# Kernel optimization log

Hardware: AMD Instinct MI355X
Metric: run time of the kernel (lower is better)

## Reference

```python
import jax, jax.numpy as jnp
import numpy as np

B, S, D, H, HD, L, V = 32, 512, 512, 8, 64, 6, 64000
EPS = 1e-5

def _layer_norm(x, g, b):
    mu = jnp.mean(x, axis=-1, keepdims=True)
    var = jnp.mean(jnp.square(x - mu), axis=-1, keepdims=True)
    return (x - mu) * jax.lax.rsqrt(var + EPS) * g + b

def _sinusoidal_pe():
    pos = np.arange(S)[:, None].astype(np.float32)
    div = np.exp(np.arange(0, D, 2).astype(np.float32) * -(np.log(10000.0) / D))
    pe = np.zeros((S, D), dtype=np.float32)
    pe[:, 0::2] = np.sin(pos * div)
    pe[:, 1::2] = np.cos(pos * div)
    return jnp.asarray(pe)

def setup_inputs() -> dict:
    key = jax.random.key(0)
    ks = jax.random.split(key, 8)
    std = 0.02
    return {
        'tokens': jax.random.randint(ks[0], (B, S), 0, V),
        'mask': jnp.ones((B, S), dtype=jnp.int32),
        'emb': jax.random.normal(ks[1], (V, D), jnp.float32) * std,
        'pe': _sinusoidal_pe(),
        'Wq': jax.random.normal(ks[2], (L, H, D, HD), jnp.float32) * std,
        'Wk': jax.random.normal(ks[3], (L, H, D, HD), jnp.float32) * std,
        'Wv': jax.random.normal(ks[4], (L, H, D, HD), jnp.float32) * std,
        'Wo': jax.random.normal(ks[5], (L, D, D), jnp.float32) * std,
        'ln1_g': jnp.ones((L, D), jnp.float32),
        'ln1_b': jnp.zeros((L, D), jnp.float32),
        'W1': jax.random.normal(ks[6], (L, D, 4 * D), jnp.float32) * std,
        'b1': jnp.zeros((L, 4 * D), jnp.float32),
        'W2': jax.random.normal(ks[7], (L, 4 * D, D), jnp.float32) * std,
        'b2': jnp.zeros((L, D), jnp.float32),
        'ln2_g': jnp.ones((L, D), jnp.float32),
        'ln2_b': jnp.zeros((L, D), jnp.float32),
    }

def reference(tokens, mask, emb, pe, Wq, Wk, Wv, Wo, ln1_g, ln1_b, W1, b1, W2, b2, ln2_g, ln2_b):
    # Eval mode: all dropouts are identity.
    x = emb[tokens] + pe[None, :S, :]               # [B,S,D]
    neg_inf = jnp.finfo(x.dtype).min
    mask_b = (mask == 0)[:, None, None, :]          # [B,1,1,S] broadcast over heads & queries
    scale = HD ** -0.5
    for l in range(L):
        q = jnp.einsum('bsd,hde->bhse', x, Wq[l])
        k = jnp.einsum('bsd,hde->bhse', x, Wk[l])
        v = jnp.einsum('bsd,hde->bhse', x, Wv[l])
        w = jnp.einsum('bhse,bhte->bhst', q, k) * scale
        w = jnp.where(mask_b, neg_inf, w)
        a = jax.nn.softmax(w, axis=-1)
        o = jnp.einsum('bhst,bhte->bhse', a, v)     # [B,H,S,HD]
        o = o.transpose(0, 2, 1, 3).reshape(x.shape[0], S, D)  # concat heads
        x = _layer_norm(x + o @ Wo[l], ln1_g[l], ln1_b[l])
        h = jax.nn.gelu(x @ W1[l] + b1[l], approximate=False) @ W2[l] + b2[l]
        x = _layer_norm(x + h, ln2_g[l], ln2_b[l])
    return x
```

## Files before the change

### kernel.cpp

```cpp
#include <hip/hip_runtime.h>

#define BB 32
#define SS 512
#define DD 512
#define HH 8
#define HDH 64
#define LL 6
#define DFF 2048
#define MM (BB*SS)

typedef __attribute__((ext_vector_type(4))) float f32x4;
typedef __attribute__((ext_vector_type(8))) short s16x8;
typedef __attribute__((ext_vector_type(4))) short s16x4;

__device__ __forceinline__ unsigned short f2bf(float f) {
    union { float f; unsigned u; } v; v.f = f;
    unsigned r = v.u + 0x7fffu + ((v.u >> 16) & 1u);
    return (unsigned short)(r >> 16);
}
__device__ __forceinline__ float bf2f(unsigned short b) {
    union { unsigned u; float f; } v; v.u = ((unsigned)b) << 16;
    return v.f;
}

__device__ __forceinline__ f32x4 mfma_bf16(s16x8 a, s16x8 b, f32x4 c) {
    asm("v_mfma_f32_16x16x32_bf16 %0, %1, %2, %0" : "+v"(c) : "v"(a), "v"(b));
    return c;
}

__device__ __forceinline__ void gload_lds16(const void* g, void* l) {
    __builtin_amdgcn_global_load_lds(
        (__attribute__((address_space(1))) void*)g,
        (__attribute__((address_space(3))) void*)l, 16, 0, 0);
}

__global__ __launch_bounds__(256) void k_conv_qkv3(const float* __restrict__ Wq,
                                                   const float* __restrict__ Wk,
                                                   const float* __restrict__ Wv,
                                                   unsigned short* __restrict__ dst) {
    int i = blockIdx.x * 256 + threadIdx.x;
    if (i >= LL*3*DD*DD) return;
    int l = i / (3*DD*DD);
    int rem = i - l*(3*DD*DD);
    int n = rem >> 9;
    int kk = rem & 511;
    int which = n >> 9;
    int h = (n >> 6) & 7, e = n & 63;
    const float* W = which == 0 ? Wq : (which == 1 ? Wk : Wv);
    dst[i] = f2bf(W[(((size_t)l*HH + h)*DD + kk)*HDH + e]);
}

__global__ __launch_bounds__(256) void k_conv_t(const float* __restrict__ src,
                                                unsigned short* __restrict__ dst,
                                                int logK, int logN) {
    int i = blockIdx.x * 256 + threadIdx.x;
    if (i >= (LL << (logK + logN))) return;
    int l = i >> (logK + logN);
    int n = (i >> logK) & ((1 << logN) - 1);
    int kk = i & ((1 << logK) - 1);
    dst[i] = f2bf(src[((size_t)l << (logK + logN)) + ((size_t)kk << logN) + n]);
}

__global__ __launch_bounds__(256) void k_embed(const int* __restrict__ tokens,
                                               const float* __restrict__ emb,
                                               const float* __restrict__ pe,
                                               float* __restrict__ x,
                                               unsigned short* __restrict__ xh) {
    int i = blockIdx.x * 256 + threadIdx.x;
    int row = i >> 7;
    int d4 = (i & 127) * 4;
    int srow = row & (SS - 1);
    int tok = tokens[row];
    f32x4 ev = *(const f32x4*)(emb + (size_t)tok*DD + d4);
    f32x4 pv = *(const f32x4*)(pe + (size_t)srow*DD + d4);
    f32x4 vv; s16x4 hv;
    #pragma unroll
    for (int j = 0; j < 4; ++j) {
        vv[j] = ev[j] + pv[j];
        hv[j] = (short)f2bf(vv[j]);
    }
    *(f32x4*)(x + (size_t)row*DD + d4) = vv;
    *(s16x4*)(xh + (size_t)row*DD + d4) = hv;
}

__global__ __launch_bounds__(128) void k_ln(const float* __restrict__ x,
                                            const float* __restrict__ y,
                                            const float* __restrict__ gg,
                                            const float* __restrict__ bb,
                                            float* __restrict__ xo,
                                            unsigned short* __restrict__ xh) {
    const int row = blockIdx.x;
    const int tid = threadIdx.x;
    __shared__ float red[4];
    f32x4 xv = *(const f32x4*)(x + (size_t)row*DD + tid*4);
    f32x4 yv = *(const f32x4*)(y + (size_t)row*DD + tid*4);
    f32x4 vv;
    #pragma unroll
    for (int j = 0; j < 4; ++j) vv[j] = xv[j] + yv[j];
    float sum = vv[0] + vv[1] + vv[2] + vv[3];
    #pragma unroll
    for (int off = 1; off < 64; off <<= 1) sum += __shfl_xor(sum, off);
    if ((tid & 63) == 0) red[tid >> 6] = sum;
    __syncthreads();
    float mu = (red[0] + red[1]) * (1.0f / 512.0f);
    float s2 = 0.0f;
    #pragma unroll
    for (int j = 0; j < 4; ++j) { float d = vv[j] - mu; s2 += d * d; }
    #pragma unroll
    for (int off = 1; off < 64; off <<= 1) s2 += __shfl_xor(s2, off);
    if ((tid & 63) == 0) red[2 + (tid >> 6)] = s2;
    __syncthreads();
    float var = (red[2] + red[3]) * (1.0f / 512.0f);
    float rs = rsqrtf(var + 1e-5f);
    f32x4 gv = *(const f32x4*)(gg + tid*4);
    f32x4 bv = *(const f32x4*)(bb + tid*4);
    f32x4 ov; s16x4 hv;
    #pragma unroll
    for (int j = 0; j < 4; ++j) {
        float o = (vv[j] - mu) * rs * gv[j] + bv[j];
        ov[j] = o;
        hv[j] = (short)f2bf(o);
    }
    *(f32x4*)(xo + (size_t)row*DD + tid*4) = ov;
    *(s16x4*)(xh + (size_t)row*DD + tid*4) = hv;
}

template<int EPI>
__global__ __launch_bounds__(256, 2) void k_gemm(
    const unsigned short* __restrict__ A, const unsigned short* __restrict__ Bt,
    unsigned short* __restrict__ ob, float* __restrict__ of,
    const float* __restrict__ bias, int N, int K, int nt)
{
    __shared__ short lds[2][2][4096];
    const int tid = threadIdx.x;
    const int lane = tid & 63;
    const int wid = tid >> 6;
    const int g = lane >> 4;
    const int t16 = lane & 15;

    int nwg = gridDim.x;
    int bid = blockIdx.x;
    int cpx = nwg >> 3;
    int swz = (bid & 7) * cpx + (bid >> 3);
    int bm = swz / nt;
    int bn = swz - bm * nt;

    const unsigned short* Ag = A  + (size_t)bm * 128 * K;
    const unsigned short* Bg = Bt + (size_t)bn * 128 * K;

    auto stage = [&](int buf, int k0) {
        #pragma unroll
        for (int i = 0; i < 2; ++i) {
            int slot = i * 256 + tid;
            int r = slot >> 2;
            int j = slot & 3;
            int js = j ^ ((r >> 1) & 3);
            size_t go = (size_t)r * K + k0 + js * 8;
            int lo = i * 2048 + wid * 512;
            gload_lds16(Ag + go, &lds[buf][0][lo]);
            gload_lds16(Bg + go, &lds[buf][1][lo]);
        }
    };

    f32x4 acc[4][4];
    #pragma unroll
    for (int a_ = 0; a_ < 4; ++a_)
        #pragma unroll
        for (int b_ = 0; b_ < 4; ++b_) acc[a_][b_] = (f32x4){0.f, 0.f, 0.f, 0.f};

    const int wm = wid >> 1, wn = wid & 1;
    stage(0, 0);
    __syncthreads();
    int nk = K >> 5;
    int buf = 0;
    for (int kt = 0; kt < nk; ++kt) {
        if (kt + 1 < nk) stage(buf ^ 1, (kt + 1) << 5);
        s16x8 af[4], bf_[4];
        #pragma unroll
        for (int mt = 0; mt < 4; ++mt) {
            int r = wm * 64 + mt * 16 + t16;
            af[mt] = *(const s16x8*)&lds[buf][0][r * 32 + ((g ^ ((r >> 1) & 3)) << 3)];
        }
        #pragma unroll
        for (int nt_ = 0; nt_ < 4; ++nt_) {
            int r = wn * 64 + nt_ * 16 + t16;
            bf_[nt_] = *(const s16x8*)&lds[buf][1][r * 32 + ((g ^ ((r >> 1) & 3)) << 3)];
        }
        #pragma unroll
        for (int mt = 0; mt < 4; ++mt)
            #pragma unroll
            for (int nt_ = 0; nt_ < 4; ++nt_)
                acc[mt][nt_] = mfma_bf16(af[mt], bf_[nt_], acc[mt][nt_]);
        __syncthreads();
        buf ^= 1;
    }

    #pragma unroll
    for (int mt = 0; mt < 4; ++mt)
        #pragma unroll
        for (int nt_ = 0; nt_ < 4; ++nt_) {
            int row0 = bm * 128 + wm * 64 + mt * 16 + g * 4;
            int col  = bn * 128 + wn * 64 + nt_ * 16 + t16;
            f32x4 v = acc[mt][nt_];
            float bv = (EPI == 2 || EPI == 3) ? bias[col] : 0.0f;
            #pragma unroll
            for (int r_ = 0; r_ < 4; ++r_) {
                size_t idx = (size_t)(row0 + r_) * N + col;
                if (EPI == 0) {
                    ob[idx] = f2bf(v[r_]);
                } else if (EPI == 1) {
                    of[idx] = v[r_];
                } else if (EPI == 2) {
                    float tv = v[r_] + bv;
                    float ge = 0.5f * tv * (1.0f + erff(tv * 0.70710678118f));
                    ob[idx] = f2bf(ge);
                } else {
                    of[idx] = v[r_] + bv;
                }
            }
        }
}

__global__ __launch_bounds__(1024, 4) void k_attn(
    const unsigned short* __restrict__ qkv, const int* __restrict__ mask,
    unsigned short* __restrict__ o)
{
    extern __shared__ short smem[];
    short* Kl = smem;
    short* Vl = smem + 32768;
    const int tid = threadIdx.x;
    const int lane = tid & 63, wid = tid >> 6;
    short* Pl = smem + 65536 + wid * 1024;
    const int b = blockIdx.x >> 3, h = blockIdx.x & 7;
    const unsigned short* base = qkv + (size_t)b * SS * 1536;
    const int qc = h * 64, kc = 512 + h * 64, vc = 1024 + h * 64;

    for (int c = tid; c < 4096; c += 1024) {
        int t = c >> 3, j = c & 7;
        s16x8 kv = *(const s16x8*)(base + (size_t)t * 1536 + kc + j * 8);
        *(s16x8*)(Kl + t * 64 + ((j ^ (t & 7)) << 3)) = kv;
    }
    {
        int unit = tid >> 1, half = tid & 1;
        int t0 = (unit >> 3) << 3, e0 = (unit & 7) << 3;
        s16x8 r0 = *(const s16x8*)(base + (size_t)(t0 + half*4 + 0) * 1536 + vc + e0);
        s16x8 r1 = *(const s16x8*)(base + (size_t)(t0 + half*4 + 1) * 1536 + vc + e0);
        s16x8 r2 = *(const s16x8*)(base + (size_t)(t0 + half*4 + 2) * 1536 + vc + e0);
        s16x8 r3 = *(const s16x8*)(base + (size_t)(t0 + half*4 + 3) * 1536 + vc + e0);
        #pragma unroll
        for (int j = 0; j < 8; ++j) {
            int e = e0 + j;
            int slot = (t0 >> 3) ^ (e & 7) ^ ((e >> 3) & 7);
            s16x4 w = (s16x4){r0[j], r1[j], r2[j], r3[j]};
            *(s16x4*)(Vl + e * 512 + (slot << 3) + (half << 2)) = w;
        }
    }
    const int g = lane >> 4, t16 = lane & 15;
    unsigned mbits = 0;
    for (int n2 = 0; n2 < 32; ++n2)
        if (mask[b * SS + n2 * 16 + t16] != 0) mbits |= (1u << n2);
    __syncthreads();

    for (int qi = 0; qi < 2; ++qi) {
        const int q0 = (wid * 2 + qi) * 16;
        s16x8 aq[2];
        #pragma unroll
        for (int ks = 0; ks < 2; ++ks)
            aq[ks] = *(const s16x8*)(base + (size_t)(q0 + t16) * 1536 + qc + ks * 32 + g * 8);

        f32x4 oacc[4];
        #pragma unroll
        for (int eo = 0; eo < 4; ++eo) oacc[eo] = (f32x4){0.f, 0.f, 0.f, 0.f};
        float mx[4] = {-3.0e38f, -3.0e38f, -3.0e38f, -3.0e38f};
        float ls[4] = {0.f, 0.f, 0.f, 0.f};

        for (int tc = 0; tc < 4; ++tc) {
            f32x4 s[8];
            #pragma unroll
            for (int n2 = 0; n2 < 8; ++n2) s[n2] = (f32x4){0.f, 0.f, 0.f, 0.f};
            #pragma unroll
            for (int n2 = 0; n2 < 8; ++n2) {
                int t = tc * 128 + n2 * 16 + t16;
                #pragma unroll
                for (int ks = 0; ks < 2; ++ks) {
                    int blk = ks * 4 + g;
                    s16x8 bk = *(const s16x8*)(Kl + t * 64 + ((blk ^ (t & 7)) << 3));
                    s[n2] = mfma_bf16(aq[ks], bk, s[n2]);
                }
            }
            #pragma unroll
            for (int n2 = 0; n2 < 8; ++n2) {
                bool val = (mbits >> (tc * 8 + n2)) & 1u;
                #pragma unroll
                for (int r_ = 0; r_ < 4; ++r_)
                    s[n2][r_] = val ? s[n2][r_] * 0.125f : -3.0e38f;
            }
            float sc[4];
            #pragma unroll
            for (int r_ = 0; r_ < 4; ++r_) {
                float m = s[0][r_];
                #pragma unroll
                for (int n2 = 1; n2 < 8; ++n2) m = fmaxf(m, s[n2][r_]);
                #pragma unroll
                for (int off = 1; off < 16; off <<= 1) m = fmaxf(m, __shfl_xor(m, off));
                float mn = fmaxf(mx[r_], m);
                sc[r_] = __expf(mx[r_] - mn);
                mx[r_] = mn;
                ls[r_] *= sc[r_];
            }
            #pragma unroll
            for (int eo = 0; eo < 4; ++eo)
                #pragma unroll
                for (int r_ = 0; r_ < 4; ++r_) oacc[eo][r_] *= sc[r_];
            #pragma unroll
            for (int n2 = 0; n2 < 8; ++n2)
                #pragma unroll
                for (int r_ = 0; r_ < 4; ++r_)
                    s[n2][r_] = __expf(s[n2][r_] - mx[r_]);
            #pragma unroll
            for (int r_ = 0; r_ < 4; ++r_) {
                float t = 0.f;
                #pragma unroll
                for (int n2 = 0; n2 < 8; ++n2) t += s[n2][r_];
                #pragma unroll
                for (int off = 1; off < 16; off <<= 1) t += __shfl_xor(t, off);
                ls[r_] += t;
            }
            #pragma unroll
            for (int c4 = 0; c4 < 2; ++c4) {
                #pragma unroll
                for (int k4 = 0; k4 < 4; ++k4) {
                    int n2 = c4 * 4 + k4;
                    #pragma unroll
                    for (int r_ = 0; r_ < 4; ++r_) {
                        int qq = g * 4 + r_;
                        int kk = k4 * 16 + t16;
                        Pl[qq * 64 + (((kk >> 3) ^ (qq & 7)) << 3) + (kk & 7)] =
                            (short)f2bf(s[n2][r_]);
                    }
                }
                #pragma unroll
                for (int ks2 = 0; ks2 < 2; ++ks2) {
                    int kk = ks2 * 32 + g * 8;
                    s16x8 pa = *(const s16x8*)(Pl + t16 * 64 + (((kk >> 3) ^ (t16 & 7)) << 3));
                    int tg = tc * 128 + c4 * 64 + kk;
                    #pragma unroll
                    for (int eo = 0; eo < 4; ++eo) {
                        int e = eo * 16 + t16;
                        int slot = (tg >> 3) ^ (e & 7) ^ ((e >> 3) & 7);
                        s16x8 bv = *(const s16x8*)(Vl + e * 512 + (slot << 3));
                        oacc[eo] = mfma_bf16(pa, bv, oacc[eo]);
                    }
                }
            }
        }
        #pragma unroll
        for (int eo = 0; eo < 4; ++eo)
            #pragma unroll
            for (int r_ = 0; r_ < 4; ++r_) {
                int row = q0 + g * 4 + r_;
                int e = eo * 16 + t16;
                o[((size_t)b * SS + row) * DD + h * HDH + e] =
                    f2bf(oacc[eo][r_] / ls[r_]);
            }
    }
}

extern "C" void kernel_launch(void* const* d_in, const int* in_sizes, int n_in,
                              void* d_out, int out_size, void* d_ws, size_t ws_size,
                              hipStream_t stream)
{
    const int*   tokens = (const int*)d_in[0];
    const int*   mask   = (const int*)d_in[1];
    const float* emb    = (const float*)d_in[2];
    const float* pe     = (const float*)d_in[3];
    const float* Wq     = (const float*)d_in[4];
    const float* Wk     = (const float*)d_in[5];
    const float* Wv     = (const float*)d_in[6];
    const float* Wo     = (const float*)d_in[7];
    const float* l1g    = (const float*)d_in[8];
    const float* l1b    = (const float*)d_in[9];
    const float* W1     = (const float*)d_in[10];
    const float* b1     = (const float*)d_in[11];
    const float* W2     = (const float*)d_in[12];
    const float* b2     = (const float*)d_in[13];
    const float* l2g    = (const float*)d_in[14];
    const float* l2b    = (const float*)d_in[15];

    char* p = (char*)d_ws;
    auto alloc = [&](size_t bytes) { char* r = p; p += (bytes + 255) & ~(size_t)255; return r; };
    unsigned short* wqkv_t = (unsigned short*)alloc((size_t)LL*3*DD*DD*2);
    unsigned short* wo_t   = (unsigned short*)alloc((size_t)LL*DD*DD*2);
    unsigned short* w1_t   = (unsigned short*)alloc((size_t)LL*DD*DFF*2);
    unsigned short* w2_t   = (unsigned short*)alloc((size_t)LL*DD*DFF*2);
    float*          x      = (float*)alloc((size_t)MM*DD*4);
    unsigned short* xh     = (unsigned short*)alloc((size_t)MM*DD*2);
    unsigned short* qkvb   = (unsigned short*)alloc((size_t)MM*1536*2);
    unsigned short* obuf   = (unsigned short*)alloc((size_t)MM*DD*2);
    float*          ybuf   = (float*)alloc((size_t)MM*DD*4);
    unsigned short* hbuf   = qkvb;

    k_conv_qkv3<<<18432, 256, 0, stream>>>(Wq, Wk, Wv, wqkv_t);
    k_conv_t<<<6144, 256, 0, stream>>>(Wo, wo_t, 9, 9);
    k_conv_t<<<24576, 256, 0, stream>>>(W1, w1_t, 9, 11);
    k_conv_t<<<24576, 256, 0, stream>>>(W2, w2_t, 11, 9);
    k_embed<<<8192, 256, 0, stream>>>(tokens, emb, pe, x, xh);

    hipFuncSetAttribute((const void*)k_attn,
                        hipFuncAttributeMaxDynamicSharedMemorySize, 163840);

    for (int l = 0; l < LL; ++l) {
        const unsigned short* wqkvl = wqkv_t + (size_t)l*3*DD*DD;
        const unsigned short* wol   = wo_t   + (size_t)l*DD*DD;
        const unsigned short* w1l   = w1_t   + (size_t)l*DD*DFF;
        const unsigned short* w2l   = w2_t   + (size_t)l*DD*DFF;

        k_gemm<0><<<1536, 256, 0, stream>>>(xh, wqkvl, qkvb, nullptr, nullptr, 1536, 512, 12);
        k_attn<<<256, 1024, 163840, stream>>>(qkvb, mask, obuf);
        k_gemm<1><<<512, 256, 0, stream>>>(obuf, wol, nullptr, ybuf, nullptr, 512, 512, 4);
        k_ln<<<16384, 128, 0, stream>>>(x, ybuf, l1g + l*DD, l1b + l*DD, x, xh);
        k_gemm<2><<<2048, 256, 0, stream>>>(xh, w1l, hbuf, nullptr, b1 + (size_t)l*DFF, 2048, 512, 16);
        k_gemm<3><<<512, 256, 0, stream>>>(hbuf, w2l, nullptr, ybuf, b2 + (size_t)l*DD, 512, 2048, 4);
        float* xout = (l == LL - 1) ? (float*)d_out : x;
        k_ln<<<16384, 128, 0, stream>>>(x, ybuf, l2g + l*DD, l2b + l*DD, xout, xh);
    }
}
```

Before: 1.504 ms.

## Rewrite GEMM with 256x128 tiles, 8 waves, and triple-buffered K=64 pipeline

Replaces the 128x128, 4-wave, double-buffered GEMM with a 256x128 tile run by 8 waves. It uses K=64 steps, a 3-slot LDS ring in dynamic shared memory, and vmcnt-based waits so two stages load ahead. The B fragment is reused across two half-passes over A, with loads for the next stage interleaved between them and MFMA priority raised. The aim is more data reuse per LDS byte and better overlap of global loads with MFMA. In exchange, 144KB of LDS per block limits occupancy to one block per CU and halves the grid, which could hurt the small N=512 GEMMs.

```diff
diff --git a/kernel.cpp b/kernel.cpp
--- a/kernel.cpp
+++ b/kernel.cpp
@@ -126,17 +126,18 @@
 }
 
 template<int EPI>
-__global__ __launch_bounds__(256, 2) void k_gemm(
+__global__ __launch_bounds__(512, 2) void k_gemm8(
     const unsigned short* __restrict__ A, const unsigned short* __restrict__ Bt,
     unsigned short* __restrict__ ob, float* __restrict__ of,
     const float* __restrict__ bias, int N, int K, int nt)
 {
-    __shared__ short lds[2][2][4096];
+    extern __shared__ short lds[];
     const int tid = threadIdx.x;
     const int lane = tid & 63;
     const int wid = tid >> 6;
     const int g = lane >> 4;
     const int t16 = lane & 15;
+    const int wm = wid >> 2, wn = wid & 3;
 
     int nwg = gridDim.x;
     int bid = blockIdx.x;
@@ -145,63 +146,105 @@
     int bm = swz / nt;
     int bn = swz - bm * nt;
 
-    const unsigned short* Ag = A  + (size_t)bm * 128 * K;
+    const unsigned short* Ag = A  + (size_t)bm * 256 * K;
     const unsigned short* Bg = Bt + (size_t)bn * 128 * K;
 
-    auto stage = [&](int buf, int k0) {
-        #pragma unroll
-        for (int i = 0; i < 2; ++i) {
-            int slot = i * 256 + tid;
-            int r = slot >> 2;
-            int j = slot & 3;
-            int js = j ^ ((r >> 1) & 3);
-            size_t go = (size_t)r * K + k0 + js * 8;
-            int lo = i * 2048 + wid * 512;
-            gload_lds16(Ag + go, &lds[buf][0][lo]);
-            gload_lds16(Bg + go, &lds[buf][1][lo]);
+    auto stage_unit = [&](int slot, int t, int unit) {
+        const int k0 = t << 6;
+        const unsigned short* src = (unit == 2) ? Bg : (Ag + (unit ? (size_t)128 * K : 0));
+        short* dst0 = lds + slot * 24576 + (unit == 2 ? 16384 : unit * 8192);
+        #pragma unroll
+        for (int rr = 0; rr < 2; ++rr) {
+            int rb = rr * 64 + wid * 8;
+            int r_in = rb + (lane >> 3);
+            int c = (lane & 7) ^ (r_in & 7);
+            gload_lds16(src + (size_t)r_in * K + k0 + c * 8, dst0 + rb * 64);
         }
     };
 
-    f32x4 acc[4][4];
-    #pragma unroll
-    for (int a_ = 0; a_ < 4; ++a_)
-        #pragma unroll
-        for (int b_ = 0; b_ < 4; ++b_) acc[a_][b_] = (f32x4){0.f, 0.f, 0.f, 0.f};
-
-    const int wm = wid >> 1, wn = wid & 1;
-    stage(0, 0);
-    __syncthreads();
-    int nk = K >> 5;
-    int buf = 0;
-    for (int kt = 0; kt < nk; ++kt) {
-        if (kt + 1 < nk) stage(buf ^ 1, (kt + 1) << 5);
-        s16x8 af[4], bf_[4];
-        #pragma unroll
-        for (int mt = 0; mt < 4; ++mt) {
-            int r = wm * 64 + mt * 16 + t16;
-            af[mt] = *(const s16x8*)&lds[buf][0][r * 32 + ((g ^ ((r >> 1) & 3)) << 3)];
-        }
-        #pragma unroll
-        for (int nt_ = 0; nt_ < 4; ++nt_) {
-            int r = wn * 64 + nt_ * 16 + t16;
-            bf_[nt_] = *(const s16x8*)&lds[buf][1][r * 32 + ((g ^ ((r >> 1) & 3)) << 3)];
-        }
-        #pragma unroll
-        for (int mt = 0; mt < 4; ++mt)
-            #pragma unroll
-            for (int nt_ = 0; nt_ < 4; ++nt_)
-                acc[mt][nt_] = mfma_bf16(af[mt], bf_[nt_], acc[mt][nt_]);
-        __syncthreads();
-        buf ^= 1;
-    }
-
-    #pragma unroll
-    for (int mt = 0; mt < 4; ++mt)
-        #pragma unroll
-        for (int nt_ = 0; nt_ < 4; ++nt_) {
-            int row0 = bm * 128 + wm * 64 + mt * 16 + g * 4;
-            int col  = bn * 128 + wn * 64 + nt_ * 16 + t16;
-            f32x4 v = acc[mt][nt_];
+    f32x4 acc[8][2];
+    #pragma unroll
+    for (int a_ = 0; a_ < 8; ++a_)
+        #pragma unroll
+        for (int b_ = 0; b_ < 2; ++b_) acc[a_][b_] = (f32x4){0.f, 0.f, 0.f, 0.f};
+
+    const int nk = K >> 6;
+    stage_unit(0, 0, 0); stage_unit(0, 0, 1); stage_unit(0, 0, 2);
+    stage_unit(1, 1, 0); stage_unit(1, 1, 1); stage_unit(1, 1, 2);
+
+    int slot = 0;
+    for (int t = 0; t < nk; ++t) {
+        if (t + 1 < nk) asm volatile("s_waitcnt vmcnt(6)" ::: "memory");
+        else            asm volatile("s_waitcnt vmcnt(0)" ::: "memory");
+        __builtin_amdgcn_s_barrier();
+        __builtin_amdgcn_sched_barrier(0);
+
+        int s2 = slot + 2; if (s2 >= 3) s2 -= 3;
+        const short* As = lds + slot * 24576;
+        const short* Bs = As + 16384;
+
+        if (t + 2 < nk) { stage_unit(s2, t + 2, 0); stage_unit(s2, t + 2, 1); }
+        s16x8 bfr[2][2];
+        #pragma unroll
+        for (int nn = 0; nn < 2; ++nn) {
+            int row = wn * 32 + nn * 16 + t16;
+            #pragma unroll
+            for (int kk = 0; kk < 2; ++kk)
+                bfr[nn][kk] = *(const s16x8*)&Bs[row * 64 + (((kk * 4 + g) ^ (row & 7)) << 3)];
+        }
+        {
+            s16x8 afr[4][2];
+            #pragma unroll
+            for (int mm = 0; mm < 4; ++mm) {
+                int row = wm * 128 + mm * 16 + t16;
+                #pragma unroll
+                for (int kk = 0; kk < 2; ++kk)
+                    afr[mm][kk] = *(const s16x8*)&As[row * 64 + (((kk * 4 + g) ^ (row & 7)) << 3)];
+            }
+            __builtin_amdgcn_sched_barrier(0);
+            __builtin_amdgcn_s_setprio(1);
+            #pragma unroll
+            for (int mm = 0; mm < 4; ++mm)
+                #pragma unroll
+                for (int nn = 0; nn < 2; ++nn)
+                    #pragma unroll
+                    for (int kk = 0; kk < 2; ++kk)
+                        acc[mm][nn] = mfma_bf16(afr[mm][kk], bfr[nn][kk], acc[mm][nn]);
+            __builtin_amdgcn_s_setprio(0);
+            __builtin_amdgcn_sched_barrier(0);
+        }
+        if (t + 2 < nk) stage_unit(s2, t + 2, 2);
+        {
+            s16x8 afr[4][2];
+            #pragma unroll
+            for (int mm = 0; mm < 4; ++mm) {
+                int row = wm * 128 + (mm + 4) * 16 + t16;
+                #pragma unroll
+                for (int kk = 0; kk < 2; ++kk)
+                    afr[mm][kk] = *(const s16x8*)&As[row * 64 + (((kk * 4 + g) ^ (row & 7)) << 3)];
+            }
+            __builtin_amdgcn_sched_barrier(0);
+            __builtin_amdgcn_s_setprio(1);
+            #pragma unroll
+            for (int mm = 0; mm < 4; ++mm)
+                #pragma unroll
+                for (int nn = 0; nn < 2; ++nn)
+                    #pragma unroll
+                    for (int kk = 0; kk < 2; ++kk)
+                        acc[mm + 4][nn] = mfma_bf16(afr[mm][kk], bfr[nn][kk], acc[mm + 4][nn]);
+            __builtin_amdgcn_s_setprio(0);
+            __builtin_amdgcn_sched_barrier(0);
+        }
+        slot = slot + 1 == 3 ? 0 : slot + 1;
+    }
+
+    #pragma unroll
+    for (int mm = 0; mm < 8; ++mm)
+        #pragma unroll
+        for (int nn = 0; nn < 2; ++nn) {
+            int row0 = bm * 256 + wm * 128 + mm * 16 + g * 4;
+            int col  = bn * 128 + wn * 32 + nn * 16 + t16;
+            f32x4 v = acc[mm][nn];
             float bv = (EPI == 2 || EPI == 3) ? bias[col] : 0.0f;
             #pragma unroll
             for (int r_ = 0; r_ < 4; ++r_) {
@@ -408,6 +451,14 @@
 
     hipFuncSetAttribute((const void*)k_attn,
                         hipFuncAttributeMaxDynamicSharedMemorySize, 163840);
+    hipFuncSetAttribute((const void*)k_gemm8<0>,
+                        hipFuncAttributeMaxDynamicSharedMemorySize, 147456);
+    hipFuncSetAttribute((const void*)k_gemm8<1>,
+                        hipFuncAttributeMaxDynamicSharedMemorySize, 147456);
+    hipFuncSetAttribute((const void*)k_gemm8<2>,
+                        hipFuncAttributeMaxDynamicSharedMemorySize, 147456);
+    hipFuncSetAttribute((const void*)k_gemm8<3>,
+                        hipFuncAttributeMaxDynamicSharedMemorySize, 147456);
 
     for (int l = 0; l < LL; ++l) {
         const unsigned short* wqkvl = wqkv_t + (size_t)l*3*DD*DD;
@@ -415,12 +466,12 @@
         const unsigned short* w1l   = w1_t   + (size_t)l*DD*DFF;
         const unsigned short* w2l   = w2_t   + (size_t)l*DD*DFF;
 
-        k_gemm<0><<<1536, 256, 0, stream>>>(xh, wqkvl, qkvb, nullptr, nullptr, 1536, 512, 12);
+        k_gemm8<0><<<768, 512, 147456, stream>>>(xh, wqkvl, qkvb, nullptr, nullptr, 1536, 512, 12);
         k_attn<<<256, 1024, 163840, stream>>>(qkvb, mask, obuf);
-        k_gemm<1><<<512, 256, 0, stream>>>(obuf, wol, nullptr, ybuf, nullptr, 512, 512, 4);
+        k_gemm8<1><<<256, 512, 147456, stream>>>(obuf, wol, nullptr, ybuf, nullptr, 512, 512, 4);
         k_ln<<<16384, 128, 0, stream>>>(x, ybuf, l1g + l*DD, l1b + l*DD, x, xh);
-        k_gemm<2><<<2048, 256, 0, stream>>>(xh, w1l, hbuf, nullptr, b1 + (size_t)l*DFF, 2048, 512, 16);
-        k_gemm<3><<<512, 256, 0, stream>>>(hbuf, w2l, nullptr, ybuf, b2 + (size_t)l*DD, 512, 2048, 4);
+        k_gemm8<2><<<1024, 512, 147456, stream>>>(xh, w1l, hbuf, nullptr, b1 + (size_t)l*DFF, 2048, 512, 16);
+        k_gemm8<3><<<256, 512, 147456, stream>>>(hbuf, w2l, nullptr, ybuf, b2 + (size_t)l*DD, 512, 2048, 4);
         float* xout = (l == LL - 1) ? (float*)d_out : x;
         k_ln<<<16384, 128, 0, stream>>>(x, ybuf, l2g + l*DD, l2b + l*DD, xout, xh);
     }
```

Result: slower. 1.580 ms (+5.0%).

## Fuse output and FFN2 GEMMs with residual add and LayerNorm

Applied to the files above, without the earlier changes.

Replaces the Wo and W2 GEMMs plus separate LayerNorm kernels with a new GEMM kernel in which each 512-thread block computes a full 64-row by 512-column output tile. It then adds bias and residual, reduces row statistics across waves through LDS, and writes normalized fp32 and bf16 outputs directly. This removes the fp32 intermediate buffer round trip and two kernel launches per layer. The cost is only 256 blocks with large per-block tiles, which lowers parallelism on a many-CU GPU. Variance is also computed in one pass as E[x^2]-mu^2, which is slightly less numerically stable.

```diff
diff --git a/kernel.cpp b/kernel.cpp
--- a/kernel.cpp
+++ b/kernel.cpp
@@ -83,52 +83,10 @@
     *(s16x4*)(xh + (size_t)row*DD + d4) = hv;
 }
 
-__global__ __launch_bounds__(128) void k_ln(const float* __restrict__ x,
-                                            const float* __restrict__ y,
-                                            const float* __restrict__ gg,
-                                            const float* __restrict__ bb,
-                                            float* __restrict__ xo,
-                                            unsigned short* __restrict__ xh) {
-    const int row = blockIdx.x;
-    const int tid = threadIdx.x;
-    __shared__ float red[4];
-    f32x4 xv = *(const f32x4*)(x + (size_t)row*DD + tid*4);
-    f32x4 yv = *(const f32x4*)(y + (size_t)row*DD + tid*4);
-    f32x4 vv;
-    #pragma unroll
-    for (int j = 0; j < 4; ++j) vv[j] = xv[j] + yv[j];
-    float sum = vv[0] + vv[1] + vv[2] + vv[3];
-    #pragma unroll
-    for (int off = 1; off < 64; off <<= 1) sum += __shfl_xor(sum, off);
-    if ((tid & 63) == 0) red[tid >> 6] = sum;
-    __syncthreads();
-    float mu = (red[0] + red[1]) * (1.0f / 512.0f);
-    float s2 = 0.0f;
-    #pragma unroll
-    for (int j = 0; j < 4; ++j) { float d = vv[j] - mu; s2 += d * d; }
-    #pragma unroll
-    for (int off = 1; off < 64; off <<= 1) s2 += __shfl_xor(s2, off);
-    if ((tid & 63) == 0) red[2 + (tid >> 6)] = s2;
-    __syncthreads();
-    float var = (red[2] + red[3]) * (1.0f / 512.0f);
-    float rs = rsqrtf(var + 1e-5f);
-    f32x4 gv = *(const f32x4*)(gg + tid*4);
-    f32x4 bv = *(const f32x4*)(bb + tid*4);
-    f32x4 ov; s16x4 hv;
-    #pragma unroll
-    for (int j = 0; j < 4; ++j) {
-        float o = (vv[j] - mu) * rs * gv[j] + bv[j];
-        ov[j] = o;
-        hv[j] = (short)f2bf(o);
-    }
-    *(f32x4*)(xo + (size_t)row*DD + tid*4) = ov;
-    *(s16x4*)(xh + (size_t)row*DD + tid*4) = hv;
-}
-
 template<int EPI>
 __global__ __launch_bounds__(256, 2) void k_gemm(
     const unsigned short* __restrict__ A, const unsigned short* __restrict__ Bt,
-    unsigned short* __restrict__ ob, float* __restrict__ of,
+    unsigned short* __restrict__ ob,
     const float* __restrict__ bias, int N, int K, int nt)
 {
     __shared__ short lds[2][2][4096];
@@ -202,21 +160,149 @@
             int row0 = bm * 128 + wm * 64 + mt * 16 + g * 4;
             int col  = bn * 128 + wn * 64 + nt_ * 16 + t16;
             f32x4 v = acc[mt][nt_];
-            float bv = (EPI == 2 || EPI == 3) ? bias[col] : 0.0f;
+            float bv = (EPI == 2) ? bias[col] : 0.0f;
             #pragma unroll
             for (int r_ = 0; r_ < 4; ++r_) {
                 size_t idx = (size_t)(row0 + r_) * N + col;
                 if (EPI == 0) {
                     ob[idx] = f2bf(v[r_]);
-                } else if (EPI == 1) {
-                    of[idx] = v[r_];
-                } else if (EPI == 2) {
+                } else {
                     float tv = v[r_] + bv;
                     float ge = 0.5f * tv * (1.0f + erff(tv * 0.70710678118f));
                     ob[idx] = f2bf(ge);
-                } else {
-                    of[idx] = v[r_] + bv;
                 }
+            }
+        }
+}
+
+template<bool HASB>
+__global__ __launch_bounds__(512, 2) void k_gemm_ln(
+    const unsigned short* __restrict__ A, const unsigned short* __restrict__ Bt,
+    const float* __restrict__ bias, const float* __restrict__ xres,
+    const float* __restrict__ gg, const float* __restrict__ bb,
+    float* __restrict__ xo, unsigned short* __restrict__ xh, int K)
+{
+    extern __shared__ short smem[];
+    const int tid = threadIdx.x;
+    const int lane = tid & 63;
+    const int wid = tid >> 6;
+    const int g = lane >> 4;
+    const int t16 = lane & 15;
+    const int bm = blockIdx.x;
+
+    const unsigned short* Ag = A + (size_t)bm * 64 * K;
+
+    auto stage = [&](int buf, int k0) {
+        short* base = smem + buf * 18432;
+        if (tid < 256) {
+            int r = tid >> 2, j = tid & 3;
+            int js = j ^ ((r >> 1) & 3);
+            gload_lds16(Ag + (size_t)r * K + k0 + js * 8, base + wid * 512 + (lane & 56) * 8 + (lane & 7) * 8);
+        }
+        #pragma unroll
+        for (int i = 0; i < 4; ++i) {
+            int slot = i * 512 + tid;
+            int r = slot >> 2, j = slot & 3;
+            int js = j ^ ((r >> 1) & 3);
+            gload_lds16(Bt + (size_t)r * K + k0 + js * 8,
+                        base + 2048 + i * 4096 + wid * 512 + lane * 8);
+        }
+    };
+
+    f32x4 acc[4][4];
+    #pragma unroll
+    for (int a_ = 0; a_ < 4; ++a_)
+        #pragma unroll
+        for (int b_ = 0; b_ < 4; ++b_) acc[a_][b_] = (f32x4){0.f, 0.f, 0.f, 0.f};
+
+    stage(0, 0);
+    __syncthreads();
+    const int nk = K >> 5;
+    int buf = 0;
+    for (int kt = 0; kt < nk; ++kt) {
+        if (kt + 1 < nk) stage(buf ^ 1, (kt + 1) << 5);
+        const short* base = smem + buf * 18432;
+        s16x8 af[4], bf_[4];
+        #pragma unroll
+        for (int mt = 0; mt < 4; ++mt) {
+            int r = mt * 16 + t16;
+            af[mt] = *(const s16x8*)&base[r * 32 + ((g ^ ((r >> 1) & 3)) << 3)];
+        }
+        #pragma unroll
+        for (int nt_ = 0; nt_ < 4; ++nt_) {
+            int r = wid * 64 + nt_ * 16 + t16;
+            bf_[nt_] = *(const s16x8*)&base[2048 + r * 32 + ((g ^ ((r >> 1) & 3)) << 3)];
+        }
+        #pragma unroll
+        for (int mt = 0; mt < 4; ++mt)
+            #pragma unroll
+            for (int nt_ = 0; nt_ < 4; ++nt_)
+                acc[mt][nt_] = mfma_bf16(af[mt], bf_[nt_], acc[mt][nt_]);
+        __syncthreads();
+        buf ^= 1;
+    }
+
+    float* pS = (float*)smem;
+    float* pQ = pS + 512;
+    float bv[4], gv[4], b2v[4];
+    #pragma unroll
+    for (int nt_ = 0; nt_ < 4; ++nt_) {
+        int col = wid * 64 + nt_ * 16 + t16;
+        bv[nt_]  = HASB ? bias[col] : 0.0f;
+        gv[nt_]  = gg[col];
+        b2v[nt_] = bb[col];
+    }
+    __syncthreads();
+    #pragma unroll
+    for (int mt = 0; mt < 4; ++mt) {
+        float xold[4][4];
+        #pragma unroll
+        for (int nt_ = 0; nt_ < 4; ++nt_) {
+            int col = wid * 64 + nt_ * 16 + t16;
+            #pragma unroll
+            for (int r_ = 0; r_ < 4; ++r_)
+                xold[nt_][r_] = xres[(size_t)(bm * 64 + mt * 16 + g * 4 + r_) * DD + col];
+        }
+        #pragma unroll
+        for (int r_ = 0; r_ < 4; ++r_) {
+            float s = 0.f, q = 0.f;
+            #pragma unroll
+            for (int nt_ = 0; nt_ < 4; ++nt_) {
+                float v = acc[mt][nt_][r_] + bv[nt_] + xold[nt_][r_];
+                acc[mt][nt_][r_] = v;
+                s += v; q += v * v;
+            }
+            #pragma unroll
+            for (int off = 1; off < 16; off <<= 1) {
+                s += __shfl_xor(s, off);
+                q += __shfl_xor(q, off);
+            }
+            if (t16 == 0) {
+                int row = mt * 16 + g * 4 + r_;
+                pS[wid * 64 + row] = s;
+                pQ[wid * 64 + row] = q;
+            }
+        }
+    }
+    __syncthreads();
+    #pragma unroll
+    for (int mt = 0; mt < 4; ++mt)
+        #pragma unroll
+        for (int r_ = 0; r_ < 4; ++r_) {
+            int row = mt * 16 + g * 4 + r_;
+            float s = 0.f, q = 0.f;
+            #pragma unroll
+            for (int w = 0; w < 8; ++w) { s += pS[w * 64 + row]; q += pQ[w * 64 + row]; }
+            float mu = s * (1.0f / 512.0f);
+            float var = q * (1.0f / 512.0f) - mu * mu;
+            float rs = rsqrtf(var + 1e-5f);
+            size_t gr = (size_t)(bm * 64 + row) * DD;
+            #pragma unroll
+            for (int nt_ = 0; nt_ < 4; ++nt_) {
+                int col = wid * 64 + nt_ * 16 + t16;
+                float o = (acc[mt][nt_][r_] - mu) * rs * gv[nt_] + b2v[nt_];
+                xo[gr + col] = o;
+                xh[gr + col] = f2bf(o);
             }
         }
 }
@@ -397,7 +483,6 @@
     unsigned short* xh     = (unsigned short*)alloc((size_t)MM*DD*2);
     unsigned short* qkvb   = (unsigned short*)alloc((size_t)MM*1536*2);
     unsigned short* obuf   = (unsigned short*)alloc((size_t)MM*DD*2);
-    float*          ybuf   = (float*)alloc((size_t)MM*DD*4);
     unsigned short* hbuf   = qkvb;
 
     k_conv_qkv3<<<18432, 256, 0, stream>>>(Wq, Wk, Wv, wqkv_t);
@@ -408,6 +493,10 @@
 
     hipFuncSetAttribute((const void*)k_attn,
                         hipFuncAttributeMaxDynamicSharedMemorySize, 163840);
+    hipFuncSetAttribute((const void*)k_gemm_ln<false>,
+                        hipFuncAttributeMaxDynamicSharedMemorySize, 73728);
+    hipFuncSetAttribute((const void*)k_gemm_ln<true>,
+                        hipFuncAttributeMaxDynamicSharedMemorySize, 73728);
 
     for (int l = 0; l < LL; ++l) {
         const unsigned short* wqkvl = wqkv_t + (size_t)l*3*DD*DD;
@@ -415,13 +504,13 @@
         const unsigned short* w1l   = w1_t   + (size_t)l*DD*DFF;
         const unsigned short* w2l   = w2_t   + (size_t)l*DD*DFF;
 
-        k_gemm<0><<<1536, 256, 0, stream>>>(xh, wqkvl, qkvb, nullptr, nullptr, 1536, 512, 12);
+        k_gemm<0><<<1536, 256, 0, stream>>>(xh, wqkvl, qkvb, nullptr, 1536, 512, 12);
         k_attn<<<256, 1024, 163840, stream>>>(qkvb, mask, obuf);
-        k_gemm<1><<<512, 256, 0, stream>>>(obuf, wol, nullptr, ybuf, nullptr, 512, 512, 4);
-        k_ln<<<16384, 128, 0, stream>>>(x, ybuf, l1g + l*DD, l1b + l*DD, x, xh);
-        k_gemm<2><<<2048, 256, 0, stream>>>(xh, w1l, hbuf, nullptr, b1 + (size_t)l*DFF, 2048, 512, 16);
-        k_gemm<3><<<512, 256, 0, stream>>>(hbuf, w2l, nullptr, ybuf, b2 + (size_t)l*DD, 512, 2048, 4);
+        k_gemm_ln<false><<<256, 512, 73728, stream>>>(
+            obuf, wol, nullptr, x, l1g + l*DD, l1b + l*DD, x, xh, 512);
+        k_gemm<2><<<2048, 256, 0, stream>>>(xh, w1l, hbuf, b1 + (size_t)l*DFF, 2048, 512, 16);
         float* xout = (l == LL - 1) ? (float*)d_out : x;
-        k_ln<<<16384, 128, 0, stream>>>(x, ybuf, l2g + l*DD, l2b + l*DD, xout, xh);
-    }
-}
+        k_gemm_ln<true><<<256, 512, 73728, stream>>>(
+            hbuf, w2l, b2 + (size_t)l*DD, x, l2g + l*DD, l2b + l*DD, xout, xh, 2048);
+    }
+}
```

New measurement: 1.547 ms. 2.9% more time.
